# Kernel tuning notes

Measured on AMD Instinct MI355X. Metric: run time of the kernel, lower is better.

Reference implementation:

```python
import jax, jax.numpy as jnp
import numpy as np

ALPHA = 0.5        # self._alpha
MAX_COEFF = 10.0   # self._max_coeff
SHARPNESS = 5      # self._loss_sharpness

N_VARS = 1_000_000
N_CLAUSES = 4_000_000
N_EDGES = 12_000_000


def setup_inputs() -> dict:
    key = jax.random.key(0)
    k1, k2, k3, k4 = jax.random.split(key, 4)
    variable_prediction = jax.random.uniform(k1, (N_VARS, 1), dtype=jnp.float32)
    lits = jax.random.randint(k2, (N_EDGES,), 0, N_VARS, dtype=jnp.int32)
    clauses = jax.random.randint(k3, (N_EDGES,), 0, N_CLAUSES, dtype=jnp.int32)
    graph_map = jnp.stack([lits, clauses])  # [2, E]
    # literal polarity: +1 (positive literal) or -1 (negated literal)
    edge_feature = jnp.where(jax.random.bernoulli(k4, 0.5, (N_EDGES, 1)), 1.0, -1.0).astype(jnp.float32)
    return {
        "variable_prediction": variable_prediction,
        "graph_map": graph_map,
        "edge_feature": edge_feature,
        "num_clauses": N_CLAUSES,
        "global_step": jnp.array([100.0], dtype=jnp.float32),
        "eps": jnp.array([1e-10], dtype=jnp.float32),
    }


def reference(variable_prediction, graph_map, edge_feature, num_clauses, global_step, eps):
    # temperature coefficient: min(step^alpha, max_coeff)
    coeff = jnp.minimum(global_step ** ALPHA, MAX_COEFF)  # [1]
    lits = graph_map[0]     # [E] variable index per edge
    clauses = graph_map[1]  # [E] clause index per edge
    ef = edge_feature[:, 0]  # [E]

    # sparse mm (signed variable mask @ prediction) == signed gather
    edge_values = ef * variable_prediction[lits, 0]          # [E]
    edge_values = edge_values + (1.0 - ef) * 0.5             # negated literal -> 1 - p
    weights = jnp.exp(coeff * edge_values)                   # [E]

    # sparse mm (function mask @ .) == scatter-add over clauses
    nominator = jax.ops.segment_sum(weights * edge_values, clauses, num_segments=num_clauses)
    denominator = jax.ops.segment_sum(weights, clauses, num_segments=num_clauses)

    clause_value = denominator / jnp.maximum(nominator, eps)
    clause_value = 1.0 + (clause_value - 1.0) ** SHARPNESS
    return jnp.mean(jnp.log(jnp.maximum(clause_value, eps)))
```

## Files before the change

kernel.cpp:

```cpp
#include <hip/hip_runtime.h>
#include <math.h>


constexpr int   N_CLAUSES_C = 4000000;
constexpr int   BKT_SHIFT   = 13;
constexpr int   BKT_CLS     = 1 << BKT_SHIFT;
constexpr int   NB_TOTAL    = (N_CLAUSES_C + BKT_CLS - 1) >> BKT_SHIFT;
constexpr int   CAP         = 25728;
constexpr int   SUB_CLS     = 4096;
constexpr int   SRT_CAP     = 13824;
constexpr int   SC_THREADS  = 1024;
constexpr int   BATCH       = 8192;
constexpr int   NBATCH      = 3;
constexpr int   SC_CHUNK    = BATCH * NBATCH;
constexpr int   PR_THREADS  = 512;

typedef int v4i __attribute__((ext_vector_type(4)));

__device__ __forceinline__ uint32_t ev_enc(float ev) {
    return (__float_as_uint(ev) + 0x800u) >> 12;
}
__device__ __forceinline__ float ev_dec(uint32_t q) {
    return __uint_as_float(q << 12);
}

__device__ __forceinline__ void load_pair(const int* __restrict__ cls,
                                          const int* __restrict__ lits,
                                          int base, int c1, int (&cc)[8], int (&ll)[8]) {
    if (base + 8 <= c1) {
        v4i ca = __builtin_nontemporal_load((const v4i*)(cls  + base));
        v4i cb = __builtin_nontemporal_load((const v4i*)(cls  + base + 4));
        v4i la = __builtin_nontemporal_load((const v4i*)(lits + base));
        v4i lb = __builtin_nontemporal_load((const v4i*)(lits + base + 4));
        #pragma unroll
        for (int i = 0; i < 4; ++i) {
            cc[i] = ca[i]; cc[4 + i] = cb[i];
            ll[i] = la[i]; ll[4 + i] = lb[i];
        }
    } else {
        #pragma unroll
        for (int i = 0; i < 8; ++i) {
            int e = base + i;
            if (e < c1) { cc[i] = cls[e]; ll[i] = lits[e]; }
            else        { cc[i] = -1;     ll[i] = 0;       }
        }
    }
}

__device__ __forceinline__ void load_ef(const int* __restrict__ efi,
                                        int base, int c1, int (&ss)[8]) {
    if (base + 8 <= c1) {
        v4i fa = __builtin_nontemporal_load((const v4i*)(efi + base));
        v4i fb = __builtin_nontemporal_load((const v4i*)(efi + base + 4));
        #pragma unroll
        for (int i = 0; i < 4; ++i) { ss[i] = fa[i]; ss[4 + i] = fb[i]; }
    } else {
        #pragma unroll
        for (int i = 0; i < 8; ++i) { int e = base + i; ss[i] = (e < c1) ? efi[e] : 0; }
    }
}

__global__ __launch_bounds__(SC_THREADS) void
scatter_kernel(const float* __restrict__ vp,
               const int* __restrict__ lits,
               const int* __restrict__ cls,
               const int* __restrict__ efi,
               uint32_t* __restrict__ payload,
               uint32_t* __restrict__ cursors,
               int n_edges, int b_lo, int b_hi) {
    __shared__ uint32_t bh[512];
    __shared__ uint32_t bOff[512];
    __shared__ uint32_t bb[512];
    __shared__ uint32_t buf[BATCH];
    __shared__ uint16_t bufB[BATCH];
    __shared__ uint32_t totalS;

    const int tid  = threadIdx.x;
    const int lane = tid & 63;
    const int wv   = tid >> 6;
    const int nbp  = b_hi - b_lo;
    const int c0   = blockIdx.x * SC_CHUNK;
    const int c1   = min(n_edges, c0 + SC_CHUNK);
    const int nb   = (c1 - c0 + BATCH - 1) / BATCH;

    int cc[8], ll[8], ss[8];
    float vv[8];
    uint32_t meta[8];

    load_pair(cls, lits, c0 + tid * 8, c1, cc, ll);
    if (tid < 512) bh[tid] = 0;
    __syncthreads();

    load_ef(efi, c0 + tid * 8, c1, ss);
    #pragma unroll
    for (int i = 0; i < 8; ++i) vv[i] = (cc[i] >= 0) ? vp[ll[i]] : 0.0f;
    #pragma unroll
    for (int i = 0; i < 8; ++i) {
        meta[i] = 0xFF800000u;
        if (cc[i] >= 0) {
            int b = cc[i] >> BKT_SHIFT;
            if (b >= b_lo && b < b_hi) {
                uint32_t ib = (uint32_t)(b - b_lo);
                uint32_t r  = atomicAdd(&bh[ib], 1u);
                if (r < 1024u)
                    meta[i] = ((uint32_t)cc[i] & 8191u) | (r << 13) | (ib << 23);
            }
        }
    }
    __syncthreads();

    for (int k = 0; k < nb; ++k) {
        if (wv == 0) {
            const int jb = lane * 8;
            uint32_t t = 0;
            #pragma unroll
            for (int i = 0; i < 8; ++i) t += bh[jb + i];
            uint32_t x = t;
            #pragma unroll
            for (int d = 1; d < 64; d <<= 1) {
                uint32_t n = __shfl_up(x, (unsigned)d, 64);
                if (lane >= d) x += n;
            }
            uint32_t run = x - t;
            #pragma unroll
            for (int i = 0; i < 8; ++i) {
                uint32_t v = bh[jb + i];
                bOff[jb + i] = run;
                run += v;
            }
            if (lane == 63) totalS = x;
        } else {
            for (int i = tid - 64; i < nbp; i += SC_THREADS - 64) {
                uint32_t v = bh[i];
                bb[i] = v ? atomicAdd(&cursors[b_lo + i], v) : 0u;
            }
        }
        __syncthreads();

        #pragma unroll
        for (int i = 0; i < 8; ++i) {
            uint32_t ib = meta[i] >> 23;
            if (ib < 511u) {
                float ev = (ss[i] >= 0) ? vv[i] : (1.0f - vv[i]);
                uint32_t s = bOff[ib] + ((meta[i] >> 13) & 1023u);
                buf[s]  = (ev_enc(ev) << BKT_SHIFT) | (meta[i] & 8191u);
                bufB[s] = (uint16_t)ib;
            }
        }
        if (tid < 512) bh[tid] = 0;
        if (k + 1 < nb)
            load_pair(cls, lits, c0 + (k + 1) * BATCH + tid * 8, c1, cc, ll);
        __syncthreads();

        if (k + 1 < nb) {
            load_ef(efi, c0 + (k + 1) * BATCH + tid * 8, c1, ss);
            #pragma unroll
            for (int i = 0; i < 8; ++i) vv[i] = (cc[i] >= 0) ? vp[ll[i]] : 0.0f;
            #pragma unroll
            for (int i = 0; i < 8; ++i) {
                meta[i] = 0xFF800000u;
                if (cc[i] >= 0) {
                    int b = cc[i] >> BKT_SHIFT;
                    if (b >= b_lo && b < b_hi) {
                        uint32_t ib = (uint32_t)(b - b_lo);
                        uint32_t r  = atomicAdd(&bh[ib], 1u);
                        if (r < 1024u)
                            meta[i] = ((uint32_t)cc[i] & 8191u) | (r << 13) | (ib << 23);
                    }
                }
            }
        }
        const uint32_t tS = totalS;
        for (uint32_t s = tid; s < tS; s += SC_THREADS) {
            uint32_t ib   = bufB[s];
            uint32_t gpos = bb[ib] + (s - bOff[ib]);
            if (gpos < (uint32_t)CAP)
                payload[(size_t)ib * CAP + gpos] = buf[s];
        }
        __syncthreads();
    }
}

__global__ __launch_bounds__(PR_THREADS) void
process_kernel(const uint32_t* __restrict__ payload,
               const uint32_t* __restrict__ cursors,
               const float* __restrict__ gstep,
               const float* __restrict__ epsp,
               double* __restrict__ acc,
               int b_lo, int nbp) {
    __shared__ uint32_t offp[SUB_CLS / 2];
    __shared__ uint32_t srt[SRT_CAP];
    __shared__ uint32_t wscan[8];
    __shared__ double   wsum[8];
    const int tid  = threadIdx.x;
    const int lane = tid & 63;
    const int wv   = tid >> 6;

    const int bid = blockIdx.x;
    const int ibc = (bid >> 4) * 8 + (bid & 7);
    const int half = (bid >> 3) & 1;
    if (ibc >= nbp) return;
    const int b = b_lo + ibc;
    const uint32_t hmask = (uint32_t)half << 12;

    for (int j = tid; j < SUB_CLS / 2; j += PR_THREADS) offp[j] = 0;
    __syncthreads();

    const uint32_t cnt = min(cursors[b], (uint32_t)CAP);
    const uint32_t* pl = payload + (size_t)ibc * CAP;
    const uint32_t nv = cnt >> 2;

    for (uint32_t k = tid; k < nv; k += PR_THREADS) {
        uint4 p4 = ((const uint4*)pl)[k];
        #pragma unroll
        for (int j = 0; j < 4; ++j) {
            uint32_t p = (j == 0) ? p4.x : (j == 1) ? p4.y : (j == 2) ? p4.z : p4.w;
            if ((p & 4096u) == hmask) {
                uint32_t c = p & 4095u;
                atomicAdd(&offp[c >> 1], 1u << ((c & 1) << 4));
            }
        }
    }
    for (uint32_t k = (nv << 2) + tid; k < cnt; k += PR_THREADS) {
        uint32_t p = pl[k];
        if ((p & 4096u) == hmask) {
            uint32_t c = p & 4095u;
            atomicAdd(&offp[c >> 1], 1u << ((c & 1) << 4));
        }
    }
    __syncthreads();

    uint32_t pk[4];
    const int jb = tid * 4;
    uint32_t t = 0;
    #pragma unroll
    for (int i = 0; i < 4; ++i) {
        pk[i] = offp[jb + i];
        t += (pk[i] & 0xFFFFu) + (pk[i] >> 16);
    }
    uint32_t x = t;
    #pragma unroll
    for (int d = 1; d < 64; d <<= 1) {
        uint32_t n = __shfl_up(x, (unsigned)d, 64);
        if (lane >= d) x += n;
    }
    if (lane == 63) wscan[wv] = x;
    __syncthreads();
    if (tid == 0) {
        uint32_t r = 0;
        #pragma unroll
        for (int w = 0; w < 8; ++w) { uint32_t tm = wscan[w]; wscan[w] = r; r += tm; }
    }
    __syncthreads();
    uint32_t run = (x - t) + wscan[wv];
    #pragma unroll
    for (int i = 0; i < 4; ++i) {
        uint32_t lo = pk[i] & 0xFFFFu, hi = pk[i] >> 16;
        offp[jb + i] = run | ((run + lo) << 16);
        run += lo + hi;
    }
    __syncthreads();

    for (uint32_t k = tid; k < nv; k += PR_THREADS) {
        uint4 p4 = ((const uint4*)pl)[k];
        #pragma unroll
        for (int j = 0; j < 4; ++j) {
            uint32_t p = (j == 0) ? p4.x : (j == 1) ? p4.y : (j == 2) ? p4.z : p4.w;
            if ((p & 4096u) == hmask) {
                uint32_t c = p & 4095u;
                uint32_t sh = (c & 1) << 4;
                uint32_t r = atomicAdd(&offp[c >> 1], 1u << sh);
                uint32_t pos = (r >> sh) & 0xFFFFu;
                if (pos < (uint32_t)SRT_CAP) srt[pos] = p;
            }
        }
    }
    for (uint32_t k = (nv << 2) + tid; k < cnt; k += PR_THREADS) {
        uint32_t p = pl[k];
        if ((p & 4096u) == hmask) {
            uint32_t c = p & 4095u;
            uint32_t sh = (c & 1) << 4;
            uint32_t r = atomicAdd(&offp[c >> 1], 1u << sh);
            uint32_t pos = (r >> sh) & 0xFFFFu;
            if (pos < (uint32_t)SRT_CAP) srt[pos] = p;
        }
    }
    __syncthreads();

    const float coeff = fminf(sqrtf(gstep[0]), 10.0f);
    const float eps   = epsp[0];
    const int gbase = (b << BKT_SHIFT) + (half << 12);
    double local = 0.0;
    for (int j = tid; j < SUB_CLS; j += PR_THREADS) {
        if (gbase + j < N_CLAUSES_C) {
            uint32_t e = (offp[j >> 1] >> ((j & 1) << 4)) & 0xFFFFu;
            uint32_t s = 0;
            if (j > 0) {
                int jm = j - 1;
                s = (offp[jm >> 1] >> ((jm & 1) << 4)) & 0xFFFFu;
            }
            e = min(e, (uint32_t)SRT_CAP);
            s = min(s, e);
            float nom = 0.f, den = 0.f;
            for (uint32_t k = s; k < e; ++k) {
                float ev = ev_dec(srt[k] >> BKT_SHIFT);
                float w  = __expf(coeff * ev);
                nom = fmaf(w, ev, nom);
                den += w;
            }
            float cv = den / fmaxf(nom, eps);
            float tt = cv - 1.0f;
            float t2 = tt * tt;
            float cv2 = 1.0f + t2 * t2 * tt;
            local += (double)__logf(fmaxf(cv2, eps));
        }
    }
    #pragma unroll
    for (int off = 32; off > 0; off >>= 1) local += __shfl_down(local, off, 64);
    if (lane == 0) wsum[wv] = local;
    __syncthreads();
    if (tid == 0) {
        double s = 0.0;
        #pragma unroll
        for (int w = 0; w < 8; ++w) s += wsum[w];
        unsafeAtomicAdd(acc, s);
    }
}

__global__ void finalize_kernel(const double* __restrict__ acc,
                                const int* __restrict__ ncp,
                                float* __restrict__ out) {
    if (threadIdx.x == 0 && blockIdx.x == 0)
        out[0] = (float)(acc[0] / (double)ncp[0]);
}

extern "C" void kernel_launch(void* const* d_in, const int* in_sizes, int n_in,
                              void* d_out, int out_size, void* d_ws, size_t ws_size,
                              hipStream_t stream) {
    const float* vp    = (const float*)d_in[0];
    const int*   gmap  = (const int*)d_in[1];
    const float* ef    = (const float*)d_in[2];
    const int*   ncp   = (const int*)d_in[3];
    const float* gstep = (const float*)d_in[4];
    const float* epsp  = (const float*)d_in[5];
    float*       out   = (float*)d_out;

    const int n_edges = in_sizes[1] / 2;
    const int* lits = gmap;
    const int* cls  = gmap + n_edges;

    int P = 8;
    int nbp_max = (NB_TOTAL + 7) / 8;
    size_t cursors_off_w = (size_t)nbp_max * CAP;
    size_t acc_off_w = (cursors_off_w + NB_TOTAL + 1) & ~(size_t)1;
    const int cands[4] = {1, 2, 4, 8};
    for (int ci = 0; ci < 4; ++ci) {
        int cand = cands[ci];
        int nm = (NB_TOTAL + cand - 1) / cand;
        size_t pw = (size_t)nm * CAP;
        size_t cw = pw + NB_TOTAL;
        size_t aw = (cw + 1) & ~(size_t)1;
        size_t need = aw * 4 + 8;
        if (need <= ws_size) { P = cand; nbp_max = nm; cursors_off_w = pw; acc_off_w = aw; break; }
    }

    uint32_t* payload = (uint32_t*)d_ws;
    uint32_t* cursors = payload + cursors_off_w;
    double*   acc     = (double*)((uint32_t*)d_ws + acc_off_w);

    hipMemsetAsync(cursors, 0, (acc_off_w - cursors_off_w) * 4 + 8, stream);

    const int sc_blocks = (n_edges + SC_CHUNK - 1) / SC_CHUNK;
    for (int p = 0; p < P; ++p) {
        int b_lo = p * nbp_max;
        int b_hi = min(NB_TOTAL, b_lo + nbp_max);
        if (b_lo >= b_hi) continue;
        int nbp = b_hi - b_lo;
        scatter_kernel<<<sc_blocks, SC_THREADS, 0, stream>>>(
            vp, lits, cls, (const int*)ef, payload, cursors, n_edges, b_lo, b_hi);
        int pr_grid = ((2 * nbp + 15) / 16) * 16;
        process_kernel<<<pr_grid, PR_THREADS, 0, stream>>>(
            payload, cursors, gstep, epsp, acc, b_lo, nbp);
    }
    finalize_kernel<<<1, 64, 0, stream>>>(acc, ncp, out);
}
```

Before: 166.5 us.

## Process each clause bucket in one 1024-thread block instead of two halves

The process kernel now handles a whole 8192-clause bucket per block with 1024 threads, sorting all bucket entries in shared memory, instead of two 512-thread blocks that each read the whole bucket payload and filter out half. This removes the duplicated payload reads and the half-mask filtering. In exchange it uses about 16K words more shared memory per block (roughly 120KB), which limits occupancy to about one block per CU, and it launches half as many blocks.

```diff
diff --git a/kernel.cpp b/kernel.cpp
--- a/kernel.cpp
+++ b/kernel.cpp
@@ -7,13 +7,11 @@
 constexpr int   BKT_CLS     = 1 << BKT_SHIFT;
 constexpr int   NB_TOTAL    = (N_CLAUSES_C + BKT_CLS - 1) >> BKT_SHIFT;
 constexpr int   CAP         = 25728;
-constexpr int   SUB_CLS     = 4096;
-constexpr int   SRT_CAP     = 13824;
 constexpr int   SC_THREADS  = 1024;
 constexpr int   BATCH       = 8192;
 constexpr int   NBATCH      = 3;
 constexpr int   SC_CHUNK    = BATCH * NBATCH;
-constexpr int   PR_THREADS  = 512;
+constexpr int   PR_THREADS  = 1024;
 
 typedef int v4i __attribute__((ext_vector_type(4)));
 
@@ -188,22 +186,18 @@
                const float* __restrict__ epsp,
                double* __restrict__ acc,
                int b_lo, int nbp) {
-    __shared__ uint32_t offp[SUB_CLS / 2];
-    __shared__ uint32_t srt[SRT_CAP];
-    __shared__ uint32_t wscan[8];
-    __shared__ double   wsum[8];
+    __shared__ uint32_t offp[BKT_CLS / 2];
+    __shared__ uint32_t srt[CAP];
+    __shared__ uint32_t wscan[16];
+    __shared__ double   wsum[16];
     const int tid  = threadIdx.x;
     const int lane = tid & 63;
     const int wv   = tid >> 6;
-
-    const int bid = blockIdx.x;
-    const int ibc = (bid >> 4) * 8 + (bid & 7);
-    const int half = (bid >> 3) & 1;
+    const int ibc  = blockIdx.x;
     if (ibc >= nbp) return;
     const int b = b_lo + ibc;
-    const uint32_t hmask = (uint32_t)half << 12;
-
-    for (int j = tid; j < SUB_CLS / 2; j += PR_THREADS) offp[j] = 0;
+
+    for (int j = tid; j < BKT_CLS / 2; j += PR_THREADS) offp[j] = 0;
     __syncthreads();
 
     const uint32_t cnt = min(cursors[b], (uint32_t)CAP);
@@ -212,21 +206,15 @@
 
     for (uint32_t k = tid; k < nv; k += PR_THREADS) {
         uint4 p4 = ((const uint4*)pl)[k];
-        #pragma unroll
-        for (int j = 0; j < 4; ++j) {
-            uint32_t p = (j == 0) ? p4.x : (j == 1) ? p4.y : (j == 2) ? p4.z : p4.w;
-            if ((p & 4096u) == hmask) {
-                uint32_t c = p & 4095u;
-                atomicAdd(&offp[c >> 1], 1u << ((c & 1) << 4));
-            }
-        }
+        uint32_t c;
+        c = p4.x & (BKT_CLS - 1); atomicAdd(&offp[c >> 1], 1u << ((c & 1) << 4));
+        c = p4.y & (BKT_CLS - 1); atomicAdd(&offp[c >> 1], 1u << ((c & 1) << 4));
+        c = p4.z & (BKT_CLS - 1); atomicAdd(&offp[c >> 1], 1u << ((c & 1) << 4));
+        c = p4.w & (BKT_CLS - 1); atomicAdd(&offp[c >> 1], 1u << ((c & 1) << 4));
     }
     for (uint32_t k = (nv << 2) + tid; k < cnt; k += PR_THREADS) {
-        uint32_t p = pl[k];
-        if ((p & 4096u) == hmask) {
-            uint32_t c = p & 4095u;
-            atomicAdd(&offp[c >> 1], 1u << ((c & 1) << 4));
-        }
+        uint32_t c = pl[k] & (BKT_CLS - 1);
+        atomicAdd(&offp[c >> 1], 1u << ((c & 1) << 4));
     }
     __syncthreads();
 
@@ -249,7 +237,7 @@
     if (tid == 0) {
         uint32_t r = 0;
         #pragma unroll
-        for (int w = 0; w < 8; ++w) { uint32_t tm = wscan[w]; wscan[w] = r; r += tm; }
+        for (int w = 0; w < 16; ++w) { uint32_t tm = wscan[w]; wscan[w] = r; r += tm; }
     }
     __syncthreads();
     uint32_t run = (x - t) + wscan[wv];
@@ -266,32 +254,28 @@
         #pragma unroll
         for (int j = 0; j < 4; ++j) {
             uint32_t p = (j == 0) ? p4.x : (j == 1) ? p4.y : (j == 2) ? p4.z : p4.w;
-            if ((p & 4096u) == hmask) {
-                uint32_t c = p & 4095u;
-                uint32_t sh = (c & 1) << 4;
-                uint32_t r = atomicAdd(&offp[c >> 1], 1u << sh);
-                uint32_t pos = (r >> sh) & 0xFFFFu;
-                if (pos < (uint32_t)SRT_CAP) srt[pos] = p;
-            }
-        }
-    }
-    for (uint32_t k = (nv << 2) + tid; k < cnt; k += PR_THREADS) {
-        uint32_t p = pl[k];
-        if ((p & 4096u) == hmask) {
-            uint32_t c = p & 4095u;
+            uint32_t c = p & (BKT_CLS - 1);
             uint32_t sh = (c & 1) << 4;
             uint32_t r = atomicAdd(&offp[c >> 1], 1u << sh);
             uint32_t pos = (r >> sh) & 0xFFFFu;
-            if (pos < (uint32_t)SRT_CAP) srt[pos] = p;
-        }
+            if (pos < (uint32_t)CAP) srt[pos] = p;
+        }
+    }
+    for (uint32_t k = (nv << 2) + tid; k < cnt; k += PR_THREADS) {
+        uint32_t p = pl[k];
+        uint32_t c = p & (BKT_CLS - 1);
+        uint32_t sh = (c & 1) << 4;
+        uint32_t r = atomicAdd(&offp[c >> 1], 1u << sh);
+        uint32_t pos = (r >> sh) & 0xFFFFu;
+        if (pos < (uint32_t)CAP) srt[pos] = p;
     }
     __syncthreads();
 
     const float coeff = fminf(sqrtf(gstep[0]), 10.0f);
     const float eps   = epsp[0];
-    const int gbase = (b << BKT_SHIFT) + (half << 12);
+    const int gbase = b << BKT_SHIFT;
     double local = 0.0;
-    for (int j = tid; j < SUB_CLS; j += PR_THREADS) {
+    for (int j = tid; j < BKT_CLS; j += PR_THREADS) {
         if (gbase + j < N_CLAUSES_C) {
             uint32_t e = (offp[j >> 1] >> ((j & 1) << 4)) & 0xFFFFu;
             uint32_t s = 0;
@@ -299,7 +283,7 @@
                 int jm = j - 1;
                 s = (offp[jm >> 1] >> ((jm & 1) << 4)) & 0xFFFFu;
             }
-            e = min(e, (uint32_t)SRT_CAP);
+            e = min(e, (uint32_t)CAP);
             s = min(s, e);
             float nom = 0.f, den = 0.f;
             for (uint32_t k = s; k < e; ++k) {
@@ -322,7 +306,7 @@
     if (tid == 0) {
         double s = 0.0;
         #pragma unroll
-        for (int w = 0; w < 8; ++w) s += wsum[w];
+        for (int w = 0; w < 16; ++w) s += wsum[w];
         unsafeAtomicAdd(acc, s);
     }
 }
@@ -378,8 +362,7 @@
         int nbp = b_hi - b_lo;
         scatter_kernel<<<sc_blocks, SC_THREADS, 0, stream>>>(
             vp, lits, cls, (const int*)ef, payload, cursors, n_edges, b_lo, b_hi);
-        int pr_grid = ((2 * nbp + 15) / 16) * 16;
-        process_kernel<<<pr_grid, PR_THREADS, 0, stream>>>(
+        process_kernel<<<nbp, PR_THREADS, 0, stream>>>(
             payload, cursors, gstep, epsp, acc, b_lo, nbp);
     }
     finalize_kernel<<<1, 64, 0, stream>>>(acc, ncp, out);
```

New measurement: 156.5 us, median of 2. 6.0% less time.
